# Optimization experiments

Hardware: AMD Instinct MI355X
Metric: run time of the kernel (lower is better)

The kernel has to match this reference:

```python
import jax, jax.numpy as jnp
import numpy as np

B, T, D = 2, 2048, 1024
H = 16
DK = D // H


def setup_inputs() -> dict:
    key = jax.random.key(0)
    ks = jax.random.split(key, 5)
    s = 1.0 / np.sqrt(D)
    return {
        "x": jax.random.normal(ks[0], (B, T, D), dtype=jnp.float32),
        "Wq": jax.random.normal(ks[1], (D, D), dtype=jnp.float32) * s,
        "bq": jnp.zeros((D,), dtype=jnp.float32),
        "Wk": jax.random.normal(ks[2], (D, D), dtype=jnp.float32) * s,
        "bk": jnp.zeros((D,), dtype=jnp.float32),
        "Wv": jax.random.normal(ks[3], (D, D), dtype=jnp.float32) * s,
        "bv": jnp.zeros((D,), dtype=jnp.float32),
        "Wo": jax.random.normal(ks[4], (D, D), dtype=jnp.float32) * s,
        "bo": jnp.zeros((D,), dtype=jnp.float32),
    }


def reference(x, Wq, bq, Wk, bk, Wv, bv, Wo, bo):
    # projections (torch Linear: x @ W.T + b; here W is stored as (in, out))
    Q = x @ Wq + bq  # (B,T,D)
    K = x @ Wk + bk
    V = x @ Wv + bv
    # split heads -> (B,H,T,dk)
    Q = Q.reshape(B, T, H, DK).transpose(0, 2, 1, 3)
    K = K.reshape(B, T, H, DK).transpose(0, 2, 1, 3)
    V = V.reshape(B, T, H, DK).transpose(0, 2, 1, 3)
    scale = 1.0 / jnp.sqrt(jnp.asarray(DK, dtype=x.dtype))
    scores = jnp.einsum("bhqd,bhkd->bhqk", Q, K) * scale  # (B,H,T,T)
    causal = jnp.tril(jnp.ones((T, T), dtype=bool))
    scores = jnp.where(causal, scores, -jnp.inf)
    weights = jax.nn.softmax(scores, axis=-1)
    # dropout is identity in eval mode
    context = jnp.einsum("bhqk,bhkd->bhqd", weights, V)
    context = context.transpose(0, 2, 1, 3).reshape(B, T, D)
    return context @ Wo + bo
```

## Files before the change

kernel.cpp:

```cpp
#include <hip/hip_runtime.h>
#include <hip/hip_bf16.h>

constexpr int Bc = 2;
constexpr int Tc = 2048;
constexpr int Mc = Bc * Tc;
constexpr float CfQ = 0.18033688011112042f;

typedef __attribute__((ext_vector_type(8))) __bf16 bf16x8;
typedef __attribute__((ext_vector_type(4))) __bf16 bf16x4;
typedef __attribute__((ext_vector_type(4))) float floatx4;

__device__ __forceinline__ void gl_lds16(const void* g, void* l) {
    __builtin_amdgcn_global_load_lds(
        (const __attribute__((address_space(1))) void*)g,
        (__attribute__((address_space(3))) void*)l, 16, 0, 0);
}

__global__ __launch_bounds__(256) void prep_all(const float* __restrict__ x,
                                                const float* __restrict__ Wq,
                                                const float* __restrict__ Wk,
                                                const float* __restrict__ Wv,
                                                const float* __restrict__ Wo,
                                                __bf16* __restrict__ xb,
                                                __bf16* __restrict__ Wqkv,
                                                __bf16* __restrict__ Wot) {
    const int z = blockIdx.z;
    const int tid = threadIdx.x;
    if (z >= 4) {
        const int lb = blockIdx.y * 16 + blockIdx.x;
        const size_t base = ((size_t)(z - 4) * 256 + lb) * 4096;
#pragma unroll
        for (int it = 0; it < 4; ++it) {
            const size_t i = base + (size_t)(it * 256 + tid) * 4;
            const float4 v = *(const float4*)(x + i);
            bf16x4 r;
            r[0] = (__bf16)v.x; r[1] = (__bf16)v.y;
            r[2] = (__bf16)v.z; r[3] = (__bf16)v.w;
            *(bf16x4*)(xb + i) = r;
        }
        return;
    }
    __shared__ float t[64][65];
    const float* W = (z == 0) ? Wq : (z == 1) ? Wk : (z == 2) ? Wv : Wo;
    __bf16* Wt = (z < 3) ? Wqkv + (size_t)z * 1024 * 1024 : Wot;
    const int k0 = blockIdx.y * 64, n0 = blockIdx.x * 64;
    const int c = tid & 63, r0 = tid >> 6;
#pragma unroll
    for (int i = 0; i < 16; ++i)
        t[r0 + i * 4][c] = W[(size_t)(k0 + r0 + i * 4) * 1024 + n0 + c];
    __syncthreads();
#pragma unroll
    for (int i = 0; i < 16; ++i) {
        const int r = r0 + i * 4;
        Wt[(size_t)(n0 + r) * 1024 + k0 + c] = (__bf16)t[c][r];
    }
}

template <int TN, bool BF16_OUT, bool FUSE_VT>
__global__ __launch_bounds__(256) void gemm_bt(const __bf16* __restrict__ A,
                                               const __bf16* __restrict__ Bt,
                                               const float* __restrict__ b0,
                                               const float* __restrict__ b1,
                                               const float* __restrict__ b2,
                                               void* __restrict__ Cv,
                                               __bf16* __restrict__ Vt,
                                               int K, int ldc) {
    constexpr int NI = TN / 32;
    __shared__ __bf16 As[128 * 64];
    __shared__ __bf16 Bs[TN * 64];
    const int tid = threadIdx.x, lane = tid & 63, wave = tid >> 6;
    const int wm = wave & 1, wn = wave >> 1;
    const int bm = blockIdx.y * 128, bn = blockIdx.x * TN;
    const __bf16* Ab = A + (size_t)bm * K;
    const __bf16* Bb = Bt + (size_t)bn * K;
    const int quad = lane >> 4, tm = lane & 15;
    const int tsw = tm & 7;

    floatx4 acc[4][NI] = {};

    for (int k0 = 0; k0 < K; k0 += 64) {
#pragma unroll
        for (int i = 0; i < 4; ++i) {
            const int s = i * 256 + tid;
            const int row = s >> 3;
            const int lc = (s & 7) ^ (row & 7);
            gl_lds16(Ab + (size_t)row * K + k0 + lc * 8, As + s * 8);
        }
#pragma unroll
        for (int i = 0; i < TN / 32; ++i) {
            const int s = i * 256 + tid;
            const int row = s >> 3;
            const int lc = (s & 7) ^ (row & 7);
            gl_lds16(Bb + (size_t)row * K + k0 + lc * 8, Bs + s * 8);
        }
        __syncthreads();
        bf16x8 af[4][2], bfv[NI][2];
#pragma unroll
        for (int mi = 0; mi < 4; ++mi) {
            const int row = (wm * 64 + mi * 16 + tm) * 64;
#pragma unroll
            for (int ks = 0; ks < 2; ++ks)
                af[mi][ks] = *(const bf16x8*)(As + row + ((ks * 4 + quad) ^ tsw) * 8);
        }
#pragma unroll
        for (int ni = 0; ni < NI; ++ni) {
            const int row = (wn * (TN / 2) + ni * 16 + tm) * 64;
#pragma unroll
            for (int ks = 0; ks < 2; ++ks)
                bfv[ni][ks] = *(const bf16x8*)(Bs + row + ((ks * 4 + quad) ^ tsw) * 8);
        }
#pragma unroll
        for (int ks = 0; ks < 2; ++ks)
#pragma unroll
            for (int mi = 0; mi < 4; ++mi)
#pragma unroll
                for (int ni = 0; ni < NI; ++ni)
                    acc[mi][ni] = __builtin_amdgcn_mfma_f32_16x16x32_bf16(
                        af[mi][ks], bfv[ni][ks], acc[mi][ni], 0, 0, 0);
        __syncthreads();
    }

#pragma unroll
    for (int ni = 0; ni < NI; ++ni) {
        const int gc = bn + wn * (TN / 2) + ni * 16 + tm;
        const float bias = (gc < 1024) ? b0[gc]
                         : (gc < 2048) ? b1[gc - 1024]
                                       : b2[gc - 2048];
        const float scale = (FUSE_VT && gc < 1024) ? CfQ : 1.0f;
#pragma unroll
        for (int mi = 0; mi < 4; ++mi) {
            const int gr0 = bm + wm * 64 + mi * 16 + quad * 4;
            if (FUSE_VT && gc >= 2048) {
                bf16x4 pv;
#pragma unroll
                for (int r = 0; r < 4; ++r) pv[r] = (__bf16)(acc[mi][ni][r] + bias);
                const int bb = gr0 >> 11, tloc = gr0 & 2047;
                const int hh = (gc - 2048) >> 6, dd = gc & 63;
                const int tperm = (tloc & ~63) + ((tloc >> 2) & 3) * 16 +
                                  ((tloc >> 4) & 3) * 4;
                *(bf16x4*)(Vt + ((size_t)(bb * 16 + hh) * 64 + dd) * 2048 + tperm) = pv;
            } else if (BF16_OUT) {
#pragma unroll
                for (int r = 0; r < 4; ++r)
                    ((__bf16*)Cv)[(size_t)(gr0 + r) * ldc + gc] =
                        (__bf16)((acc[mi][ni][r] + bias) * scale);
            } else {
#pragma unroll
                for (int r = 0; r < 4; ++r)
                    ((float*)Cv)[(size_t)(gr0 + r) * ldc + gc] =
                        acc[mi][ni][r] + bias;
            }
        }
    }
}

__global__ __launch_bounds__(512, 4) void attn_mfma(const __bf16* __restrict__ QK,
                                                    const __bf16* __restrict__ Vt,
                                                    __bf16* __restrict__ ctx) {
    constexpr float NEG = -1e30f;

    __shared__ __bf16 Ks[2][2][64 * 64];
    __shared__ __bf16 Vts[2][2][64 * 64];

    const int tid = threadIdx.x, lane = tid & 63, w = tid >> 6;
    const int g = w >> 2, wq = w & 3;
    const int c = lane & 15, quad = lane >> 4;
    const int bh = blockIdx.y, b = bh >> 4, h = bh & 15;
    const int ip = blockIdx.x;

    const __bf16* Qb = QK + (size_t)(b * Tc) * 2048 + h * 64;
    const __bf16* Kb = Qb + 1024;
    const __bf16* Vtb = Vt + (size_t)bh * 64 * 2048;

    const int sw = c & 7;
    int koff0[4], koff1[4];
#pragma unroll
    for (int ni = 0; ni < 4; ++ni) {
        const int krow = ni * 16 + c;
        koff0[ni] = krow * 64 + (quad ^ sw) * 8;
        koff1[ni] = krow * 64 + ((4 + quad) ^ sw) * 8;
    }
    int voff[4][2];
#pragma unroll
    for (int di = 0; di < 4; ++di) {
        const int vrow = di * 16 + c;
#pragma unroll
        for (int pr = 0; pr < 2; ++pr)
            voff[di][pr] = vrow * 64 + ((quad * 2 + pr) ^ sw) * 8;
    }

    const int srow = tid >> 3;
    const int slc = (tid & 7) ^ (srow & 7);
    const __bf16* kgB = Kb + (size_t)srow * 2048 + slc * 8;
    const __bf16* vgB = Vtb + (size_t)srow * 2048 + slc * 8;

#pragma unroll 1
    for (int ph = 0; ph < 2; ++ph) {
        const int qt = ph ? 31 - ip : ip;
        const int nk = qt + 1;
        const int npair = (nk + 1) >> 1;

        const __bf16* qr = Qb + (size_t)(qt * 64 + wq * 16 + c) * 2048;
        const bf16x8 qf0 = *(const bf16x8*)(qr + quad * 8);
        const bf16x8 qf1 = *(const bf16x8*)(qr + 32 + quad * 8);

        floatx4 lacc = {};
        floatx4 oa[4] = {};

        gl_lds16(kgB, &Ks[0][0][tid * 8]);
        gl_lds16(kgB + (size_t)64 * 2048, &Ks[0][1][tid * 8]);
        gl_lds16(vgB, &Vts[0][0][tid * 8]);
        gl_lds16(vgB + 64, &Vts[0][1][tid * 8]);
        __syncthreads();

        const __bf16* kg = kgB + (size_t)128 * 2048;
        const __bf16* vg = vgB + 128;

        for (int kp = 0; kp < npair; ++kp) {
            const int buf = kp & 1;
            if (kp + 1 < npair) {
                __bf16* kd = &Ks[buf ^ 1][0][tid * 8];
                __bf16* vd = &Vts[buf ^ 1][0][tid * 8];
                gl_lds16(kg, kd);
                gl_lds16(kg + (size_t)64 * 2048, kd + 4096);
                gl_lds16(vg, vd);
                gl_lds16(vg + 64, vd + 4096);
                kg += (size_t)128 * 2048;
                vg += 128;
            }
            const int kt = 2 * kp + g;
            if (kt < nk) {
                const __bf16* ks = Ks[buf][g];
                const __bf16* vs = Vts[buf][g];

                float sv[4][4];
#pragma unroll
                for (int ni = 0; ni < 4; ++ni) {
                    const bf16x8 kb0 = *(const bf16x8*)(ks + koff0[ni]);
                    const bf16x8 kb1 = *(const bf16x8*)(ks + koff1[ni]);
                    floatx4 a = {};
                    a = __builtin_amdgcn_mfma_f32_16x16x32_bf16(kb0, qf0, a, 0, 0, 0);
                    a = __builtin_amdgcn_mfma_f32_16x16x32_bf16(kb1, qf1, a, 0, 0, 0);
#pragma unroll
                    for (int r = 0; r < 4; ++r) sv[ni][r] = a[r];
                }

                if (kt == qt) {
#pragma unroll
                    for (int ni = 0; ni < 4; ++ni)
#pragma unroll
                        for (int r = 0; r < 4; ++r)
                            if (ni * 16 + quad * 4 + r > wq * 16 + c) sv[ni][r] = NEG;
                }
#pragma unroll
                for (int ni = 0; ni < 4; ++ni) {
#pragma unroll
                    for (int r = 0; r < 4; ++r) sv[ni][r] = __builtin_exp2f(sv[ni][r]);
                    lacc[0] += sv[ni][0];
                    lacc[1] += sv[ni][1];
                    lacc[2] += sv[ni][2];
                    lacc[3] += sv[ni][3];
                }

                bf16x8 pb[2];
#pragma unroll
                for (int pr = 0; pr < 2; ++pr)
#pragma unroll
                    for (int j = 0; j < 4; ++j) {
                        pb[pr][j] = (__bf16)sv[pr * 2][j];
                        pb[pr][4 + j] = (__bf16)sv[pr * 2 + 1][j];
                    }

#pragma unroll
                for (int di = 0; di < 4; ++di) {
#pragma unroll
                    for (int pr = 0; pr < 2; ++pr) {
                        const bf16x8 vf = *(const bf16x8*)(vs + voff[di][pr]);
                        oa[di] = __builtin_amdgcn_mfma_f32_16x16x32_bf16(
                            vf, pb[pr], oa[di], 0, 0, 0);
                    }
                }
            }
            __syncthreads();
        }

        float lsum = lacc[0] + lacc[1] + lacc[2] + lacc[3];
        float* sc = (float*)&Ks[0][0][0];
        if (g == 1) {
#pragma unroll
            for (int di = 0; di < 4; ++di)
                *(floatx4*)(sc + wq * 1088 + di * 256 + lane * 4) = oa[di];
            sc[wq * 1088 + 1024 + lane] = lsum;
        }
        __syncthreads();
        if (g == 0) {
#pragma unroll
            for (int di = 0; di < 4; ++di)
                oa[di] += *(const floatx4*)(sc + wq * 1088 + di * 256 + lane * 4);
            lsum += sc[wq * 1088 + 1024 + lane];
            lsum += __shfl_xor(lsum, 16);
            lsum += __shfl_xor(lsum, 32);
            const float inv = 1.f / lsum;
            __bf16* cp = ctx + (size_t)(b * Tc + qt * 64 + wq * 16 + c) * 1024 +
                         h * 64 + quad * 4;
#pragma unroll
            for (int di = 0; di < 4; ++di) {
                bf16x4 rv;
#pragma unroll
                for (int r = 0; r < 4; ++r) rv[r] = (__bf16)(oa[di][r] * inv);
                *(bf16x4*)(cp + di * 16) = rv;
            }
        }
        __syncthreads();
    }
}

extern "C" void kernel_launch(void* const* d_in, const int* in_sizes, int n_in,
                              void* d_out, int out_size, void* d_ws, size_t ws_size,
                              hipStream_t stream) {
    const float* x  = (const float*)d_in[0];
    const float* Wq = (const float*)d_in[1];
    const float* bq = (const float*)d_in[2];
    const float* Wk = (const float*)d_in[3];
    const float* bk = (const float*)d_in[4];
    const float* Wv = (const float*)d_in[5];
    const float* bv = (const float*)d_in[6];
    const float* Wo = (const float*)d_in[7];
    const float* bo = (const float*)d_in[8];

    __bf16* xb   = (__bf16*)d_ws;
    __bf16* Wqkv = xb + (size_t)Mc * 1024;
    __bf16* Wot  = Wqkv + (size_t)3072 * 1024;
    __bf16* QKb  = Wot + (size_t)1024 * 1024;
    __bf16* Vtw  = QKb + (size_t)Mc * 2048;
    __bf16* ctxb = xb;

    prep_all<<<dim3(16, 16, 8), 256, 0, stream>>>(x, Wq, Wk, Wv, Wo,
                                                  xb, Wqkv, Wot);

    gemm_bt<128, true, true><<<dim3(24, 32), 256, 0, stream>>>(
        xb, Wqkv, bq, bk, bv, QKb, Vtw, 1024, 2048);

    attn_mfma<<<dim3(16, 32), 512, 0, stream>>>(QKb, Vtw, ctxb);

    gemm_bt<64, false, false><<<dim3(16, 32), 256, 0, stream>>>(
        ctxb, Wot, bo, bo, bo, d_out, nullptr, 1024, 1024);
}
```

Before: 188.4 us.

## Deepen attention K/V prefetch with vmcnt waits, priority hints, and XCD-aware block mapping

The attention kernel now issues loads two tiles ahead, waiting with explicit s_waitcnt vmcnt counts and raw s_barrier instead of a full __syncthreads after each tile. MFMA sections are wrapped in s_setprio so waves doing math get issue priority. The grid is flattened to 1D and remapped so consecutive block IDs spread (batch, head) pairs across XCDs, aiming for better L2 locality of K/V. The aim is to hide global-load latency and cut barrier stalls. The trade-off is reliance on exact vmcnt accounting, which could break if the compiler reorders or adds memory ops.

```diff
diff --git a/kernel.cpp b/kernel.cpp
--- a/kernel.cpp
+++ b/kernel.cpp
@@ -165,8 +165,10 @@
     const int tid = threadIdx.x, lane = tid & 63, w = tid >> 6;
     const int g = w >> 2, wq = w & 3;
     const int c = lane & 15, quad = lane >> 4;
-    const int bh = blockIdx.y, b = bh >> 4, h = bh & 15;
-    const int ip = blockIdx.x;
+    const int n = blockIdx.x;
+    const int bh = (n & 7) * 4 + ((n >> 3) & 3);
+    const int ip = n >> 5;
+    const int b = bh >> 4, h = bh & 15;
 
     const __bf16* Qb = QK + (size_t)(b * Tc) * 2048 + h * 64;
     const __bf16* Kb = Qb + 1024;
@@ -207,33 +209,37 @@
         floatx4 lacc = {};
         floatx4 oa[4] = {};
 
-        gl_lds16(kgB, &Ks[0][0][tid * 8]);
-        gl_lds16(kgB + (size_t)64 * 2048, &Ks[0][1][tid * 8]);
-        gl_lds16(vgB, &Vts[0][0][tid * 8]);
-        gl_lds16(vgB + 64, &Vts[0][1][tid * 8]);
-        __syncthreads();
-
-        const __bf16* kg = kgB + (size_t)128 * 2048;
-        const __bf16* vg = vgB + 128;
+        auto stage = [&](int p, int sbuf) {
+            const __bf16* kg = kgB + (size_t)(2 * p) * 64 * 2048;
+            const __bf16* vg = vgB + 2 * p * 64;
+            __bf16* kd = &Ks[sbuf][0][tid * 8];
+            __bf16* vd = &Vts[sbuf][0][tid * 8];
+            gl_lds16(kg, kd);
+            gl_lds16(kg + (size_t)64 * 2048, kd + 4096);
+            gl_lds16(vg, vd);
+            gl_lds16(vg + 64, vd + 4096);
+        };
+
+        stage(0, 0);
+        if (npair > 1) stage(1, 1);
 
         for (int kp = 0; kp < npair; ++kp) {
             const int buf = kp & 1;
             if (kp + 1 < npair) {
-                __bf16* kd = &Ks[buf ^ 1][0][tid * 8];
-                __bf16* vd = &Vts[buf ^ 1][0][tid * 8];
-                gl_lds16(kg, kd);
-                gl_lds16(kg + (size_t)64 * 2048, kd + 4096);
-                gl_lds16(vg, vd);
-                gl_lds16(vg + 64, vd + 4096);
-                kg += (size_t)128 * 2048;
-                vg += 128;
+                asm volatile("s_waitcnt vmcnt(4)" ::: "memory");
+            } else {
+                asm volatile("s_waitcnt vmcnt(0)" ::: "memory");
             }
+            __builtin_amdgcn_sched_barrier(0);
+            __builtin_amdgcn_s_barrier();
+
             const int kt = 2 * kp + g;
             if (kt < nk) {
                 const __bf16* ks = Ks[buf][g];
                 const __bf16* vs = Vts[buf][g];
 
                 float sv[4][4];
+                __builtin_amdgcn_s_setprio(1);
 #pragma unroll
                 for (int ni = 0; ni < 4; ++ni) {
                     const bf16x8 kb0 = *(const bf16x8*)(ks + koff0[ni]);
@@ -244,6 +250,7 @@
 #pragma unroll
                     for (int r = 0; r < 4; ++r) sv[ni][r] = a[r];
                 }
+                __builtin_amdgcn_s_setprio(0);
 
                 if (kt == qt) {
 #pragma unroll
@@ -271,6 +278,7 @@
                         pb[pr][4 + j] = (__bf16)sv[pr * 2 + 1][j];
                     }
 
+                __builtin_amdgcn_s_setprio(1);
 #pragma unroll
                 for (int di = 0; di < 4; ++di) {
 #pragma unroll
@@ -280,10 +288,14 @@
                             vf, pb[pr], oa[di], 0, 0, 0);
                     }
                 }
+                __builtin_amdgcn_s_setprio(0);
             }
-            __syncthreads();
-        }
-
+            __builtin_amdgcn_sched_barrier(0);
+            __builtin_amdgcn_s_barrier();
+            if (kp + 2 < npair) stage(kp + 2, buf);
+        }
+
+        __syncthreads();
         float lsum = lacc[0] + lacc[1] + lacc[2] + lacc[3];
         float* sc = (float*)&Ks[0][0][0];
         if (g == 1) {
@@ -341,7 +353,7 @@
     gemm_bt<128, true, true><<<dim3(24, 32), 256, 0, stream>>>(
         xb, Wqkv, bq, bk, bv, QKb, Vtw, 1024, 2048);
 
-    attn_mfma<<<dim3(16, 32), 512, 0, stream>>>(QKb, Vtw, ctxb);
+    attn_mfma<<<dim3(512), 512, 0, stream>>>(QKb, Vtw, ctxb);
 
     gemm_bt<64, false, false><<<dim3(16, 32), 256, 0, stream>>>(
         ctxb, Wot, bo, bo, bo, d_out, nullptr, 1024, 1024);
```

New measurement: 179.8 us. 1.05x faster.
